# Performance work log

Measured on AMD Instinct MI355X. Metric: run time of the kernel, lower is better.

Reference implementation:

```python
import jax, jax.numpy as jnp
import numpy as np

B, S, D = 2, 2048, 512
P, T, MAP_H = 13, 5, 64


def setup_inputs() -> dict:
    key = jax.random.key(0)
    ks = jax.random.split(key, 8)
    s = 0.02
    return {
        "hidden_states": jax.random.normal(ks[0], (B, S, D), jnp.float32),
        "ln_gamma": jnp.ones((D,), jnp.float32),
        "ln_beta": jnp.zeros((D,), jnp.float32),
        "W_in": jax.random.normal(ks[1], (D, P * D), jnp.float32) * s,
        "b_in": jnp.zeros((P * D,), jnp.float32),
        "W_map1": jax.random.normal(ks[2], (D, MAP_H), jnp.float32) * s,
        "b_map1": jnp.zeros((MAP_H,), jnp.float32),
        "W_map2": jax.random.normal(ks[3], (MAP_H, T), jnp.float32) * s,
        "b_map2": jnp.zeros((T,), jnp.float32),
        "log_tau": jnp.linspace(0.0, 4.0, T).astype(jnp.float32),
        "mix": jax.random.normal(ks[4], (P, T), jnp.float32) / float(P * T),
        "W_out": jax.random.normal(ks[5], (D, D), jnp.float32) * s,
        "b_out": jnp.zeros((D,), jnp.float32),
        "scale": jnp.float32(1e-3),
        "h_prev": jnp.zeros((B, P, T, D), jnp.float32),
        "position_offset": 0,
    }


def _forward(hidden_states, ln_gamma, ln_beta, W_in, b_in, W_map1, b_map1,
             W_map2, b_map2, log_tau, mix, W_out, b_out, scale, h_prev):
    b, s_len, d = hidden_states.shape
    p, t = mix.shape
    # pre-norm (LayerNorm, eps=1e-5)
    mu = jnp.mean(hidden_states, -1, keepdims=True)
    var = jnp.var(hidden_states, -1, keepdims=True)
    xn = (hidden_states - mu) * jax.lax.rsqrt(var + 1e-5) * ln_gamma + ln_beta
    # per-protofilament input drive: [B,S,P,D]
    u = (xn @ W_in + b_in).reshape(b, s_len, p, d)
    # liquid (input-dependent) decay per time scale: [B,S,T]
    gate = jax.nn.sigmoid(jnp.tanh(xn @ W_map1 + b_map1) @ W_map2 + b_map2)
    alpha = jnp.exp(-gate / jnp.exp(log_tau))  # [B,S,T]

    def step(h, inp):
        u_t, a_t = inp                      # [B,P,D], [B,T]
        a = a_t[:, None, :, None]           # broadcast over P and D
        h = a * h + (1.0 - a) * u_t[:, :, None, :]   # [B,P,T,D]
        y = jnp.einsum('bptd,pt->bd', h, mix)        # mix protofilaments/time scales
        return h, y

    _, ys = jax.lax.scan(step, h_prev,
                         (jnp.moveaxis(u, 1, 0), jnp.moveaxis(alpha, 1, 0)))
    mt_out = jnp.moveaxis(ys, 0, 1) @ W_out + b_out  # [B,S,D]
    return hidden_states + scale * mt_out


def reference(hidden_states, ln_gamma, ln_beta, W_in, b_in, W_map1, b_map1,
              W_map2, b_map2, log_tau, mix, W_out, b_out, scale, h_prev,
              position_offset):
    return _forward(hidden_states, ln_gamma, ln_beta, W_in, b_in, W_map1,
                    b_map1, W_map2, b_map2, log_tau, mix, W_out, b_out,
                    scale, h_prev)
```

## Files before the change

### kernel.cpp

```cpp
#include <hip/hip_runtime.h>
#include <hip/hip_bf16.h>
#include <stdint.h>

#define BB 2
#define SS 2048
#define DD 512
#define PP 13
#define TT 5
#define MH 64
#define MM (BB*SS)
#define NV (TT*DD)
#define KK 512
#define CHUNK 16
#define NCH (SS/CHUNK)

typedef __attribute__((ext_vector_type(4))) float f32x4;
typedef __attribute__((ext_vector_type(8))) short s8v;
typedef unsigned int u32;
typedef __attribute__((address_space(3))) u32 lds_u32_t;
typedef __attribute__((address_space(1))) const u32 glb_u32_t;

__device__ __forceinline__ float bf2f(unsigned short u){
  union { unsigned int i; float f; } c; c.i = ((unsigned int)u) << 16; return c.f;
}
__device__ __forceinline__ unsigned short f2bf(float f){
  union { float f; unsigned int i; } c; c.f = f;
  unsigned int x = c.i;
  unsigned int r = (x + 0x7fffu + ((x >> 16) & 1u)) >> 16;
  return (unsigned short)r;
}
__device__ __forceinline__ void gld16(unsigned short* l, const unsigned short* g){
  __builtin_amdgcn_global_load_lds((glb_u32_t*)g, (lds_u32_t*)l, 16, 0, 0);
}

__global__ __launch_bounds__(256) void k_prep_ln(
    const float* __restrict__ hs,
    const float* __restrict__ gamma, const float* __restrict__ beta,
    const float* __restrict__ W_in, const float* __restrict__ b_in,
    const float* __restrict__ mix,  const float* __restrict__ W_out,
    const float* __restrict__ W1,
    unsigned short* __restrict__ xn_bf,
    unsigned short* __restrict__ W_vT, float* __restrict__ b_v,
    unsigned short* __restrict__ W_outT, unsigned short* __restrict__ W1T)
{
  int blk = blockIdx.x;
  if (blk < 1024){
    int tid = threadIdx.x;
    int lane = tid & 63;
    int row = blk*4 + (tid>>6);
    const float* x = hs + (size_t)row*DD + lane*8;
    float4 v0 = *(const float4*)x;
    float4 v1 = *(const float4*)(x+4);
    float s  = v0.x+v0.y+v0.z+v0.w + v1.x+v1.y+v1.z+v1.w;
    float sq = v0.x*v0.x+v0.y*v0.y+v0.z*v0.z+v0.w*v0.w
             + v1.x*v1.x+v1.y*v1.y+v1.z*v1.z+v1.w*v1.w;
    #pragma unroll
    for (int o=32;o>0;o>>=1){ s += __shfl_xor(s,o); sq += __shfl_xor(sq,o); }
    float mu   = s  * (1.f/DD);
    float var  = sq * (1.f/DD) - mu*mu;
    float rstd = rsqrtf(var + 1e-5f);
    float4 g0 = *(const float4*)(gamma + lane*8);
    float4 g1 = *(const float4*)(gamma + lane*8 + 4);
    float4 b0 = *(const float4*)(beta  + lane*8);
    float4 b1 = *(const float4*)(beta  + lane*8 + 4);
    union { unsigned short us[8]; uint4 u; } pk;
    pk.us[0] = f2bf((v0.x-mu)*rstd*g0.x + b0.x);
    pk.us[1] = f2bf((v0.y-mu)*rstd*g0.y + b0.y);
    pk.us[2] = f2bf((v0.z-mu)*rstd*g0.z + b0.z);
    pk.us[3] = f2bf((v0.w-mu)*rstd*g0.w + b0.w);
    pk.us[4] = f2bf((v1.x-mu)*rstd*g1.x + b1.x);
    pk.us[5] = f2bf((v1.y-mu)*rstd*g1.y + b1.y);
    pk.us[6] = f2bf((v1.z-mu)*rstd*g1.z + b1.z);
    pk.us[7] = f2bf((v1.w-mu)*rstd*g1.w + b1.w);
    *(uint4*)(xn_bf + (size_t)row*DD + lane*8) = pk.u;
  } else if (blk < 1152){
    int idx = (blk-1024) * 256 + threadIdx.x;
    int d  = idx & (DD-1);
    int k0 = idx >> 9;
    float mx[PP][TT];
    #pragma unroll
    for (int p=0;p<PP;++p)
      #pragma unroll
      for (int t=0;t<TT;++t) mx[p][t] = mix[p*TT+t];
    float acc[TT][8];
    #pragma unroll
    for (int t=0;t<TT;++t)
      #pragma unroll
      for (int j=0;j<8;++j) acc[t][j] = 0.f;
    #pragma unroll
    for (int j=0;j<8;++j){
      int k = k0*8 + j;
      const float* wrow = W_in + (size_t)k * (PP*DD) + d;
      #pragma unroll
      for (int p=0;p<PP;++p){
        float w = wrow[p*DD];
        #pragma unroll
        for (int t=0;t<TT;++t) acc[t][j] += mx[p][t]*w;
      }
    }
    #pragma unroll
    for (int t=0;t<TT;++t){
      union { unsigned short us[8]; uint4 u; } pk;
      #pragma unroll
      for (int j=0;j<8;++j) pk.us[j] = f2bf(acc[t][j]);
      *(uint4*)(W_vT + ((size_t)(t*DD+d))*KK + k0*8) = pk.u;
    }
    if (k0 == 0){
      #pragma unroll
      for (int t=0;t<TT;++t){
        float s = 0.f;
        #pragma unroll
        for (int p=0;p<PP;++p) s += mx[p][t]*b_in[p*DD+d];
        b_v[t*DD+d] = s;
      }
    }
  } else if (blk < 1280){
    int idx = (blk-1152)*256 + threadIdx.x;
    int n  = idx & (DD-1);
    int k0 = idx >> 9;
    union { unsigned short us[8]; uint4 u; } pk;
    #pragma unroll
    for (int j=0;j<8;++j) pk.us[j] = f2bf(W_out[(size_t)(k0*8+j)*DD + n]);
    *(uint4*)(W_outT + (size_t)n*KK + k0*8) = pk.u;
  } else {
    int idx = (blk-1280)*256 + threadIdx.x;
    int n  = idx >> 6;
    int k0 = idx & 63;
    union { unsigned short us[8]; uint4 u; } pk;
    #pragma unroll
    for (int j=0;j<8;++j) pk.us[j] = f2bf(W1[(size_t)(k0*8+j)*MH + n]);
    *(uint4*)(W1T + (size_t)n*KK + k0*8) = pk.u;
  }
}

__global__ __launch_bounds__(256) void k_gate(
    const unsigned short* __restrict__ xn,
    const unsigned short* __restrict__ W1T,
    const float* __restrict__ b1, const float* __restrict__ W2,
    const float* __restrict__ b2, const float* __restrict__ ltau,
    float* __restrict__ alpha)
{
  __shared__ unsigned short lA[2][64*32];
  __shared__ unsigned short lB[2][64*32];
  int bm = blockIdx.x;
  int tid = threadIdx.x, lane = tid & 63, w = tid >> 6;
  int lr = lane & 15, kq = lane >> 4;
  const uint8_t* gA = (const uint8_t*)(xn  + (size_t)(bm*64 + w*16 + (lane>>2))*KK) + (lane&3)*16;
  const uint8_t* gB = (const uint8_t*)(W1T + (size_t)(        w*16 + (lane>>2))*KK) + (lane&3)*16;
  f32x4 acc[4];
  #pragma unroll
  for (int ni=0;ni<4;++ni) acc[ni] = (f32x4){0.f,0.f,0.f,0.f};

  auto stage = [&](int buf, int kt){
    int off = kt*64;
    gld16(&lA[buf][(w*16)*32], (const unsigned short*)(gA + off));
    gld16(&lB[buf][(w*16)*32], (const unsigned short*)(gB + off));
  };
  auto compute = [&](int buf){
    union { uint4 u; s8v v; } af, bfr[4];
    af.u = *(const uint4*)&lA[buf][(w*16+lr)*32 + kq*8];
    #pragma unroll
    for (int ni=0;ni<4;++ni) bfr[ni].u = *(const uint4*)&lB[buf][(ni*16+lr)*32 + kq*8];
    #pragma unroll
    for (int ni=0;ni<4;++ni)
      acc[ni] = __builtin_amdgcn_mfma_f32_16x16x32_bf16(af.v, bfr[ni].v, acc[ni], 0,0,0);
  };

  stage(0, 0);
  __syncthreads();
  #pragma unroll
  for (int kt=1; kt<16; ++kt){
    stage(kt&1, kt);
    compute((kt&1)^1);
    __syncthreads();
  }
  compute(1);

  float z1[4][4];
  #pragma unroll
  for (int ni=0;ni<4;++ni){
    float bb = b1[ni*16+lr];
    #pragma unroll
    for (int r=0;r<4;++r) z1[r][ni] = tanhf(acc[ni][r] + bb);
  }
  float et[TT];
  #pragma unroll
  for (int t=0;t<TT;++t) et[t] = expf(-ltau[t]);
  float a[4][TT];
  #pragma unroll
  for (int t=0;t<TT;++t){
    float w2[4];
    #pragma unroll
    for (int ni=0;ni<4;++ni) w2[ni] = W2[(ni*16+lr)*TT + t];
    #pragma unroll
    for (int r=0;r<4;++r){
      float p = z1[r][0]*w2[0] + z1[r][1]*w2[1] + z1[r][2]*w2[2] + z1[r][3]*w2[3];
      #pragma unroll
      for (int o=8;o>0;o>>=1) p += __shfl_xor(p, o);
      float z2 = p + b2[t];
      float gate = 1.f/(1.f + expf(-z2));
      a[r][t] = expf(-gate * et[t]);
    }
  }
  if (lr < TT){
    int t = lr;
    #pragma unroll
    for (int r=0;r<4;++r){
      int row = bm*64 + w*16 + kq*4 + r;
      alpha[(size_t)row*TT + t] = a[r][t];
    }
  }
}

template<int BN, int NDIM, bool OUTEPI>
__global__ __launch_bounds__(256) void k_gemm(
    const unsigned short* __restrict__ A,
    const unsigned short* __restrict__ Bt,
    const float* __restrict__ bias,
    const float* __restrict__ hidden,
    const float* __restrict__ scale_p,
    float* __restrict__ outF,
    unsigned short* __restrict__ outBf)
{
  constexpr int NI  = (BN == 128) ? 4 : 2;
  constexpr int WNT = BN / 2;
  __shared__ unsigned short lA[2][128*32];
  __shared__ unsigned short lB[2][BN*32];
  int bn = blockIdx.x, bm = blockIdx.y;
  int tid  = threadIdx.x;
  int lane = tid & 63;
  int w    = tid >> 6;
  int wm = w >> 1, wn = w & 1;
  f32x4 acc[4][NI];
  #pragma unroll
  for (int i=0;i<4;++i)
    #pragma unroll
    for (int j=0;j<NI;++j) acc[i][j] = (f32x4){0.f,0.f,0.f,0.f};

  const uint8_t* gA = (const uint8_t*)(A + (size_t)(bm*128 + w*32 + (lane>>2))*KK) + (lane&3)*16;
  const uint8_t* gB;
  if constexpr (BN == 128) gB = (const uint8_t*)(Bt + (size_t)(bn*BN + w*32 + (lane>>2))*KK) + (lane&3)*16;
  else                     gB = (const uint8_t*)(Bt + (size_t)(bn*BN + w*16 + (lane>>2))*KK) + (lane&3)*16;
  int lr = lane & 15, kq = lane >> 4;

  auto stage = [&](int buf, int kt){
    int off = kt*64;
    gld16(&lA[buf][(w*32)*32],    (const unsigned short*)(gA + off));
    gld16(&lA[buf][(w*32+16)*32], (const unsigned short*)(gA + (size_t)16*KK*2 + off));
    if constexpr (BN == 128){
      gld16(&lB[buf][(w*32)*32],    (const unsigned short*)(gB + off));
      gld16(&lB[buf][(w*32+16)*32], (const unsigned short*)(gB + (size_t)16*KK*2 + off));
    } else {
      gld16(&lB[buf][(w*16)*32],    (const unsigned short*)(gB + off));
    }
  };
  auto compute = [&](int buf){
    union { uint4 u; s8v v; } af[4], bfr[NI];
    #pragma unroll
    for (int mi=0;mi<4;++mi) af[mi].u  = *(const uint4*)&lA[buf][(wm*64+mi*16+lr)*32 + kq*8];
    #pragma unroll
    for (int ni=0;ni<NI;++ni) bfr[ni].u = *(const uint4*)&lB[buf][(wn*WNT+ni*16+lr)*32 + kq*8];
    #pragma unroll
    for (int mi=0;mi<4;++mi)
      #pragma unroll
      for (int ni=0;ni<NI;++ni)
        acc[mi][ni] = __builtin_amdgcn_mfma_f32_16x16x32_bf16(af[mi].v, bfr[ni].v, acc[mi][ni], 0,0,0);
  };

  stage(0, 0);
  __syncthreads();
  #pragma unroll
  for (int kt=1; kt<16; ++kt){
    stage(kt&1, kt);
    compute((kt&1)^1);
    __syncthreads();
  }
  compute(1);

  float sc = 0.f;
  if constexpr (OUTEPI) sc = *scale_p;
  #pragma unroll
  for (int mi=0;mi<4;++mi){
    #pragma unroll
    for (int ni=0;ni<NI;++ni){
      int row = bm*128 + wm*64 + mi*16 + kq*4;
      int col = bn*BN  + wn*WNT + ni*16 + lr;
      float bs = bias[col];
      f32x4 c = acc[mi][ni];
      #pragma unroll
      for (int r=0;r<4;++r){
        float val = c[r] + bs;
        size_t off = (size_t)(row+r)*NDIM + col;
        if constexpr (OUTEPI) outF[off] = hidden[off] + sc*val;
        else                  outBf[off] = f2bf(val);
      }
    }
  }
}

__global__ __launch_bounds__(320) void k_scan_a(
    const float* __restrict__ alpha,
    unsigned short* __restrict__ vg,
    float* __restrict__ L, float* __restrict__ PA)
{
  int blk = blockIdx.x;
  int c = blk & (NCH-1), b = blk >> 7;
  int tid = threadIdx.x;
  int t  = tid >> 6;
  int d8 = tid & 63;
  __shared__ float sAl[CHUNK*TT];
  if (tid < CHUNK*TT) sAl[tid] = alpha[(size_t)(b*SS + c*CHUNK)*TT + tid];
  __syncthreads();
  unsigned short* vp = vg + (size_t)(b*SS + c*CHUNK)*NV + t*DD + d8*8;
  uint4 vv[CHUNK];
  #pragma unroll
  for (int s2=0;s2<CHUNK;++s2) vv[s2] = *(const uint4*)(vp + (size_t)s2*NV);
  float g[8];
  #pragma unroll
  for (int j=0;j<8;++j) g[j] = 0.f;
  float pa = 1.f;
  #pragma unroll
  for (int s2=0;s2<CHUNK;++s2){
    float a = sAl[s2*TT+t], om = 1.f - a;
    const unsigned short* pv = (const unsigned short*)&vv[s2];
    union { unsigned short us[8]; uint4 u; } o;
    #pragma unroll
    for (int j=0;j<8;++j){ g[j] = a*g[j] + om*bf2f(pv[j]); o.us[j] = f2bf(g[j]); }
    *(uint4*)(vp + (size_t)s2*NV) = o.u;
    pa *= a;
  }
  float* Lp = L + ((size_t)(b*TT+t)*NCH + c)*DD + d8*8;
  *(float4*)Lp     = (float4){g[0],g[1],g[2],g[3]};
  *(float4*)(Lp+4) = (float4){g[4],g[5],g[6],g[7]};
  if (d8 == 0) PA[(size_t)(b*TT+t)*NCH + c] = pa;
}

__global__ __launch_bounds__(512) void k_scan_b(
    const float* __restrict__ mix,
    const float* __restrict__ h_prev,
    const float* __restrict__ PA,
    const float* __restrict__ L,
    float* __restrict__ Gc)
{
  int blk = blockIdx.x;
  int t = blk % TT, b = blk / TT;
  int d = threadIdx.x;
  __shared__ float sP[NCH];
  if (d < NCH) sP[d] = PA[(size_t)(b*TT+t)*NCH + d];
  __syncthreads();
  float carry = 0.f;
  #pragma unroll
  for (int p=0;p<PP;++p)
    carry += mix[p*TT+t] * h_prev[((size_t)(b*PP+p)*TT + t)*DD + d];
  const float* Lp = L  + (size_t)(b*TT+t)*NCH*DD + d;
  float*       gc = Gc + (size_t)(b*TT+t)*NCH*DD + d;
  float buf[8], nbuf[8];
  #pragma unroll
  for (int j=0;j<8;++j) buf[j] = Lp[(size_t)j*DD];
  for (int c0=0;c0<NCH;c0+=8){
    if (c0+8 < NCH){
      #pragma unroll
      for (int j=0;j<8;++j) nbuf[j] = Lp[(size_t)(c0+8+j)*DD];
    }
    #pragma unroll
    for (int j=0;j<8;++j){
      gc[(size_t)(c0+j)*DD] = carry;
      carry = sP[c0+j]*carry + buf[j];
    }
    #pragma unroll
    for (int j=0;j<8;++j) buf[j] = nbuf[j];
  }
}

__global__ __launch_bounds__(256) void k_scan_c(
    const float* __restrict__ alpha,
    const unsigned short* __restrict__ g_loc,
    const float* __restrict__ Gc,
    unsigned short* __restrict__ ybf)
{
  int blk = blockIdx.x;
  int c = blk & (NCH-1), b = blk >> 7;
  int tid = threadIdx.x;
  int s4 = tid >> 6;
  int d8 = tid & 63;
  __shared__ float sAl[CHUNK*TT];
  if (tid < CHUNK*TT) sAl[tid] = alpha[(size_t)(b*SS + c*CHUNK)*TT + tid];
  __syncthreads();
  float ca[TT][8];
  #pragma unroll
  for (int t=0;t<TT;++t){
    const float* gp = Gc + ((size_t)(b*TT+t)*NCH + c)*DD + d8*8;
    float4 c0 = *(const float4*)gp;
    float4 c1 = *(const float4*)(gp+4);
    ca[t][0]=c0.x; ca[t][1]=c0.y; ca[t][2]=c0.z; ca[t][3]=c0.w;
    ca[t][4]=c1.x; ca[t][5]=c1.y; ca[t][6]=c1.z; ca[t][7]=c1.w;
  }
  float pr[TT];
  #pragma unroll
  for (int t=0;t<TT;++t){
    float p = 1.f;
    for (int j=0;j<s4*4;++j) p *= sAl[j*TT+t];
    pr[t] = p;
  }
  const unsigned short* gl = g_loc + (size_t)(b*SS + c*CHUNK)*NV + d8*8;
  unsigned short* yp = ybf + (size_t)(b*SS + c*CHUNK)*DD + d8*8;
  #pragma unroll
  for (int i=0;i<4;++i){
    int s2 = s4*4 + i;
    float y[8];
    #pragma unroll
    for (int j=0;j<8;++j) y[j] = 0.f;
    #pragma unroll
    for (int t=0;t<TT;++t){
      pr[t] *= sAl[s2*TT+t];
      uint4 gv = *(const uint4*)(gl + (size_t)s2*NV + t*DD);
      const unsigned short* gp = (const unsigned short*)&gv;
      #pragma unroll
      for (int j=0;j<8;++j) y[j] += bf2f(gp[j]) + pr[t]*ca[t][j];
    }
    union { unsigned short us[8]; uint4 u; } o;
    #pragma unroll
    for (int j=0;j<8;++j) o.us[j] = f2bf(y[j]);
    *(uint4*)(yp + (size_t)s2*DD) = o.u;
  }
}

extern "C" void kernel_launch(void* const* d_in, const int* in_sizes, int n_in,
                              void* d_out, int out_size, void* d_ws, size_t ws_size,
                              hipStream_t stream)
{
  (void)in_sizes; (void)n_in; (void)out_size; (void)ws_size;
  const float* hs     = (const float*)d_in[0];
  const float* gamma  = (const float*)d_in[1];
  const float* beta   = (const float*)d_in[2];
  const float* W_in   = (const float*)d_in[3];
  const float* b_in   = (const float*)d_in[4];
  const float* W1     = (const float*)d_in[5];
  const float* b1     = (const float*)d_in[6];
  const float* W2     = (const float*)d_in[7];
  const float* b2     = (const float*)d_in[8];
  const float* ltau   = (const float*)d_in[9];
  const float* mix    = (const float*)d_in[10];
  const float* W_out  = (const float*)d_in[11];
  const float* b_out  = (const float*)d_in[12];
  const float* scale  = (const float*)d_in[13];
  const float* h_prev = (const float*)d_in[14];
  float* out = (float*)d_out;

  uint8_t* w = (uint8_t*)d_ws;
  unsigned short* xn   = (unsigned short*)(w);
  unsigned short* WvT  = (unsigned short*)(w + 4194304);
  unsigned short* WoT  = (unsigned short*)(w + 6815744);
  float* alphaB        = (float*)(w + 7340032);
  float* b_v           = (float*)(w + 7421952);
  float* PA            = (float*)(w + 7432192);
  float* L             = (float*)(w + 7437312);
  float* Gc            = (float*)(w + 10058752);
  unsigned short* vg   = (unsigned short*)(w + 12680192);
  unsigned short* ybf  = (unsigned short*)(w + 33651712);
  unsigned short* W1T  = ybf;

  hipLaunchKernelGGL(k_prep_ln, dim3(1296), dim3(256), 0, stream,
                     hs, gamma, beta, W_in, b_in, mix, W_out, W1,
                     xn, WvT, b_v, WoT, W1T);
  hipLaunchKernelGGL(k_gate, dim3(MM/64), dim3(256), 0, stream, xn, W1T, b1, W2, b2, ltau, alphaB);
  hipLaunchKernelGGL((k_gemm<128,NV,false>), dim3(NV/128, MM/128), dim3(256), 0, stream,
                     xn, WvT, b_v, nullptr, nullptr, nullptr, vg);
  hipLaunchKernelGGL(k_scan_a, dim3(BB*NCH), dim3(320), 0, stream, alphaB, vg, L, PA);
  hipLaunchKernelGGL(k_scan_b, dim3(BB*TT), dim3(512), 0, stream, mix, h_prev, PA, L, Gc);
  hipLaunchKernelGGL(k_scan_c, dim3(BB*NCH), dim3(256), 0, stream, alphaB, vg, Gc, ybf);
  hipLaunchKernelGGL((k_gemm<64,DD,true>), dim3(DD/64, MM/128), dim3(256), 0, stream,
                     ybf, WoT, b_out, hs, scale, out, nullptr);
}
```

Before: 82.95 us.

## Fuse gate MLP into input GEMM and pre-reduce scan outputs over time scales

The separate gate kernel is removed. Its first layer (W1) is appended as extra columns of the input-drive weight matrix, zero-padded to a multiple of 128. The last column-block of the big GEMM then computes tanh, the second layer, sigmoid and alpha in its epilogue. Separately, scan_a now sums the five time-scale local states in LDS and writes a single bf16 row per position, so scan_c reads one row instead of five, cutting global traffic. This saves one launch and a pass over xn, at the cost of extra zero-padded GEMM work, an LDS buffer in scan_a, and extra syncs.

```diff
diff --git a/kernel.cpp b/kernel.cpp
--- a/kernel.cpp
+++ b/kernel.cpp
@@ -10,6 +10,7 @@
 #define MH 64
 #define MM (BB*SS)
 #define NV (TT*DD)
+#define NX 2688
 #define KK 512
 #define CHUNK 16
 #define NCH (SS/CHUNK)
@@ -38,10 +39,10 @@
     const float* __restrict__ gamma, const float* __restrict__ beta,
     const float* __restrict__ W_in, const float* __restrict__ b_in,
     const float* __restrict__ mix,  const float* __restrict__ W_out,
-    const float* __restrict__ W1,
+    const float* __restrict__ W1,   const float* __restrict__ b1,
     unsigned short* __restrict__ xn_bf,
     unsigned short* __restrict__ W_vT, float* __restrict__ b_v,
-    unsigned short* __restrict__ W_outT, unsigned short* __restrict__ W1T)
+    unsigned short* __restrict__ W_outT)
 {
   int blk = blockIdx.x;
   if (blk < 1024){
@@ -62,16 +63,16 @@
     float4 g0 = *(const float4*)(gamma + lane*8);
     float4 g1 = *(const float4*)(gamma + lane*8 + 4);
     float4 b0 = *(const float4*)(beta  + lane*8);
-    float4 b1 = *(const float4*)(beta  + lane*8 + 4);
+    float4 b1v = *(const float4*)(beta + lane*8 + 4);
     union { unsigned short us[8]; uint4 u; } pk;
     pk.us[0] = f2bf((v0.x-mu)*rstd*g0.x + b0.x);
     pk.us[1] = f2bf((v0.y-mu)*rstd*g0.y + b0.y);
     pk.us[2] = f2bf((v0.z-mu)*rstd*g0.z + b0.z);
     pk.us[3] = f2bf((v0.w-mu)*rstd*g0.w + b0.w);
-    pk.us[4] = f2bf((v1.x-mu)*rstd*g1.x + b1.x);
-    pk.us[5] = f2bf((v1.y-mu)*rstd*g1.y + b1.y);
-    pk.us[6] = f2bf((v1.z-mu)*rstd*g1.z + b1.z);
-    pk.us[7] = f2bf((v1.w-mu)*rstd*g1.w + b1.w);
+    pk.us[4] = f2bf((v1.x-mu)*rstd*g1.x + b1v.x);
+    pk.us[5] = f2bf((v1.y-mu)*rstd*g1.y + b1v.y);
+    pk.us[6] = f2bf((v1.z-mu)*rstd*g1.z + b1v.z);
+    pk.us[7] = f2bf((v1.w-mu)*rstd*g1.w + b1v.w);
     *(uint4*)(xn_bf + (size_t)row*DD + lane*8) = pk.u;
   } else if (blk < 1152){
     int idx = (blk-1024) * 256 + threadIdx.x;
@@ -122,97 +123,26 @@
     #pragma unroll
     for (int j=0;j<8;++j) pk.us[j] = f2bf(W_out[(size_t)(k0*8+j)*DD + n]);
     *(uint4*)(W_outT + (size_t)n*KK + k0*8) = pk.u;
-  } else {
+  } else if (blk < 1296){
     int idx = (blk-1280)*256 + threadIdx.x;
     int n  = idx >> 6;
     int k0 = idx & 63;
     union { unsigned short us[8]; uint4 u; } pk;
     #pragma unroll
     for (int j=0;j<8;++j) pk.us[j] = f2bf(W1[(size_t)(k0*8+j)*MH + n]);
-    *(uint4*)(W1T + (size_t)n*KK + k0*8) = pk.u;
-  }
-}
-
-__global__ __launch_bounds__(256) void k_gate(
-    const unsigned short* __restrict__ xn,
-    const unsigned short* __restrict__ W1T,
-    const float* __restrict__ b1, const float* __restrict__ W2,
-    const float* __restrict__ b2, const float* __restrict__ ltau,
-    float* __restrict__ alpha)
-{
-  __shared__ unsigned short lA[2][64*32];
-  __shared__ unsigned short lB[2][64*32];
-  int bm = blockIdx.x;
-  int tid = threadIdx.x, lane = tid & 63, w = tid >> 6;
-  int lr = lane & 15, kq = lane >> 4;
-  const uint8_t* gA = (const uint8_t*)(xn  + (size_t)(bm*64 + w*16 + (lane>>2))*KK) + (lane&3)*16;
-  const uint8_t* gB = (const uint8_t*)(W1T + (size_t)(        w*16 + (lane>>2))*KK) + (lane&3)*16;
-  f32x4 acc[4];
-  #pragma unroll
-  for (int ni=0;ni<4;++ni) acc[ni] = (f32x4){0.f,0.f,0.f,0.f};
-
-  auto stage = [&](int buf, int kt){
-    int off = kt*64;
-    gld16(&lA[buf][(w*16)*32], (const unsigned short*)(gA + off));
-    gld16(&lB[buf][(w*16)*32], (const unsigned short*)(gB + off));
-  };
-  auto compute = [&](int buf){
-    union { uint4 u; s8v v; } af, bfr[4];
-    af.u = *(const uint4*)&lA[buf][(w*16+lr)*32 + kq*8];
-    #pragma unroll
-    for (int ni=0;ni<4;++ni) bfr[ni].u = *(const uint4*)&lB[buf][(ni*16+lr)*32 + kq*8];
-    #pragma unroll
-    for (int ni=0;ni<4;++ni)
-      acc[ni] = __builtin_amdgcn_mfma_f32_16x16x32_bf16(af.v, bfr[ni].v, acc[ni], 0,0,0);
-  };
-
-  stage(0, 0);
-  __syncthreads();
-  #pragma unroll
-  for (int kt=1; kt<16; ++kt){
-    stage(kt&1, kt);
-    compute((kt&1)^1);
-    __syncthreads();
-  }
-  compute(1);
-
-  float z1[4][4];
-  #pragma unroll
-  for (int ni=0;ni<4;++ni){
-    float bb = b1[ni*16+lr];
-    #pragma unroll
-    for (int r=0;r<4;++r) z1[r][ni] = tanhf(acc[ni][r] + bb);
-  }
-  float et[TT];
-  #pragma unroll
-  for (int t=0;t<TT;++t) et[t] = expf(-ltau[t]);
-  float a[4][TT];
-  #pragma unroll
-  for (int t=0;t<TT;++t){
-    float w2[4];
-    #pragma unroll
-    for (int ni=0;ni<4;++ni) w2[ni] = W2[(ni*16+lr)*TT + t];
-    #pragma unroll
-    for (int r=0;r<4;++r){
-      float p = z1[r][0]*w2[0] + z1[r][1]*w2[1] + z1[r][2]*w2[2] + z1[r][3]*w2[3];
-      #pragma unroll
-      for (int o=8;o>0;o>>=1) p += __shfl_xor(p, o);
-      float z2 = p + b2[t];
-      float gate = 1.f/(1.f + expf(-z2));
-      a[r][t] = expf(-gate * et[t]);
-    }
-  }
-  if (lr < TT){
-    int t = lr;
-    #pragma unroll
-    for (int r=0;r<4;++r){
-      int row = bm*64 + w*16 + kq*4 + r;
-      alpha[(size_t)row*TT + t] = a[r][t];
-    }
-  }
-}
-
-template<int BN, int NDIM, bool OUTEPI>
+    *(uint4*)(W_vT + (size_t)(NV+n)*KK + k0*8) = pk.u;
+    if (k0 == 0) b_v[NV+n] = b1[n];
+  } else {
+    int idx = (blk-1296)*256 + threadIdx.x;
+    int n  = idx >> 6;
+    int k0 = idx & 63;
+    uint4 z; z.x=z.y=z.z=z.w=0u;
+    *(uint4*)(W_vT + (size_t)(NV+MH+n)*KK + k0*8) = z;
+    if (blk == 1296 && threadIdx.x < MH) b_v[NV+MH+threadIdx.x] = 0.f;
+  }
+}
+
+template<int BN, int NDIM, bool OUTEPI, bool GATE>
 __global__ __launch_bounds__(256) void k_gemm(
     const unsigned short* __restrict__ A,
     const unsigned short* __restrict__ Bt,
@@ -220,7 +150,11 @@
     const float* __restrict__ hidden,
     const float* __restrict__ scale_p,
     float* __restrict__ outF,
-    unsigned short* __restrict__ outBf)
+    unsigned short* __restrict__ outBf,
+    const float* __restrict__ W2,
+    const float* __restrict__ b2,
+    const float* __restrict__ ltau,
+    float* __restrict__ alphaOut)
 {
   constexpr int NI  = (BN == 128) ? 4 : 2;
   constexpr int WNT = BN / 2;
@@ -277,6 +211,46 @@
   }
   compute(1);
 
+  if constexpr (GATE){
+    if (bn == (int)gridDim.x - 1){
+      if (wn != 0) return;
+      float et[TT];
+      #pragma unroll
+      for (int t=0;t<TT;++t) et[t] = expf(-ltau[t]);
+      #pragma unroll
+      for (int mi=0;mi<4;++mi){
+        float z1v[4][4];
+        #pragma unroll
+        for (int ni=0;ni<4;++ni){
+          float bb = bias[bn*BN + ni*16 + lr];
+          #pragma unroll
+          for (int r=0;r<4;++r) z1v[ni][r] = tanhf(acc[mi][ni][r] + bb);
+        }
+        #pragma unroll
+        for (int t=0;t<TT;++t){
+          float w2v[4];
+          #pragma unroll
+          for (int ni=0;ni<4;++ni) w2v[ni] = W2[(ni*16+lr)*TT + t];
+          #pragma unroll
+          for (int r=0;r<4;++r){
+            float p = z1v[0][r]*w2v[0] + z1v[1][r]*w2v[1]
+                    + z1v[2][r]*w2v[2] + z1v[3][r]*w2v[3];
+            p += __shfl_xor(p, 1);
+            p += __shfl_xor(p, 2);
+            p += __shfl_xor(p, 4);
+            p += __shfl_xor(p, 8);
+            if (lr == t){
+              float gate = 1.f/(1.f + expf(-(p + b2[t])));
+              int row = bm*128 + wm*64 + mi*16 + kq*4 + r;
+              alphaOut[(size_t)row*TT + t] = expf(-gate * et[t]);
+            }
+          }
+        }
+      }
+      return;
+    }
+  }
+
   float sc = 0.f;
   if constexpr (OUTEPI) sc = *scale_p;
   #pragma unroll
@@ -300,8 +274,9 @@
 
 __global__ __launch_bounds__(320) void k_scan_a(
     const float* __restrict__ alpha,
-    unsigned short* __restrict__ vg,
-    float* __restrict__ L, float* __restrict__ PA)
+    const unsigned short* __restrict__ v,
+    float* __restrict__ L, float* __restrict__ PA,
+    unsigned short* __restrict__ yloc)
 {
   int blk = blockIdx.x;
   int c = blk & (NCH-1), b = blk >> 7;
@@ -309,25 +284,51 @@
   int t  = tid >> 6;
   int d8 = tid & 63;
   __shared__ float sAl[CHUNK*TT];
+  __shared__ unsigned short yl[TT][8][DD];
   if (tid < CHUNK*TT) sAl[tid] = alpha[(size_t)(b*SS + c*CHUNK)*TT + tid];
   __syncthreads();
-  unsigned short* vp = vg + (size_t)(b*SS + c*CHUNK)*NV + t*DD + d8*8;
-  uint4 vv[CHUNK];
-  #pragma unroll
-  for (int s2=0;s2<CHUNK;++s2) vv[s2] = *(const uint4*)(vp + (size_t)s2*NV);
+  const unsigned short* vp = v + (size_t)(b*SS + c*CHUNK)*NV + t*DD + d8*8;
   float g[8];
   #pragma unroll
   for (int j=0;j<8;++j) g[j] = 0.f;
   float pa = 1.f;
   #pragma unroll
-  for (int s2=0;s2<CHUNK;++s2){
-    float a = sAl[s2*TT+t], om = 1.f - a;
-    const unsigned short* pv = (const unsigned short*)&vv[s2];
-    union { unsigned short us[8]; uint4 u; } o;
-    #pragma unroll
-    for (int j=0;j<8;++j){ g[j] = a*g[j] + om*bf2f(pv[j]); o.us[j] = f2bf(g[j]); }
-    *(uint4*)(vp + (size_t)s2*NV) = o.u;
-    pa *= a;
+  for (int half=0; half<2; ++half){
+    uint4 vv[8];
+    #pragma unroll
+    for (int s=0;s<8;++s) vv[s] = *(const uint4*)(vp + (size_t)(half*8+s)*NV);
+    #pragma unroll
+    for (int s=0;s<8;++s){
+      float a = sAl[(half*8+s)*TT+t], om = 1.f - a;
+      const unsigned short* pv = (const unsigned short*)&vv[s];
+      union { unsigned short us[8]; uint4 u; } o;
+      #pragma unroll
+      for (int j=0;j<8;++j){ g[j] = a*g[j] + om*bf2f(pv[j]); o.us[j] = f2bf(g[j]); }
+      *(uint4*)&yl[t][s][d8*8] = o.u;
+      pa *= a;
+    }
+    __syncthreads();
+    if (t < 4){
+      #pragma unroll
+      for (int ii=0; ii<2; ++ii){
+        int s = t*2 + ii;
+        float y[8];
+        #pragma unroll
+        for (int j=0;j<8;++j) y[j] = 0.f;
+        #pragma unroll
+        for (int tt=0;tt<TT;++tt){
+          uint4 gv = *(const uint4*)&yl[tt][s][d8*8];
+          const unsigned short* gp = (const unsigned short*)&gv;
+          #pragma unroll
+          for (int j=0;j<8;++j) y[j] += bf2f(gp[j]);
+        }
+        union { unsigned short us[8]; uint4 u; } o;
+        #pragma unroll
+        for (int j=0;j<8;++j) o.us[j] = f2bf(y[j]);
+        *(uint4*)(yloc + (size_t)(b*SS + c*CHUNK + half*8 + s)*DD + d8*8) = o.u;
+      }
+    }
+    __syncthreads();
   }
   float* Lp = L + ((size_t)(b*TT+t)*NCH + c)*DD + d8*8;
   *(float4*)Lp     = (float4){g[0],g[1],g[2],g[3]};
@@ -374,7 +375,7 @@
 
 __global__ __launch_bounds__(256) void k_scan_c(
     const float* __restrict__ alpha,
-    const unsigned short* __restrict__ g_loc,
+    const unsigned short* __restrict__ yloc,
     const float* __restrict__ Gc,
     unsigned short* __restrict__ ybf)
 {
@@ -402,26 +403,26 @@
     for (int j=0;j<s4*4;++j) p *= sAl[j*TT+t];
     pr[t] = p;
   }
-  const unsigned short* gl = g_loc + (size_t)(b*SS + c*CHUNK)*NV + d8*8;
-  unsigned short* yp = ybf + (size_t)(b*SS + c*CHUNK)*DD + d8*8;
+  const unsigned short* yp = yloc + (size_t)(b*SS + c*CHUNK)*DD + d8*8;
+  unsigned short* op = ybf + (size_t)(b*SS + c*CHUNK)*DD + d8*8;
   #pragma unroll
   for (int i=0;i<4;++i){
     int s2 = s4*4 + i;
+    uint4 yv = *(const uint4*)(yp + (size_t)s2*DD);
+    const unsigned short* yq = (const unsigned short*)&yv;
     float y[8];
     #pragma unroll
-    for (int j=0;j<8;++j) y[j] = 0.f;
+    for (int j=0;j<8;++j) y[j] = bf2f(yq[j]);
     #pragma unroll
     for (int t=0;t<TT;++t){
       pr[t] *= sAl[s2*TT+t];
-      uint4 gv = *(const uint4*)(gl + (size_t)s2*NV + t*DD);
-      const unsigned short* gp = (const unsigned short*)&gv;
-      #pragma unroll
-      for (int j=0;j<8;++j) y[j] += bf2f(gp[j]) + pr[t]*ca[t][j];
+      #pragma unroll
+      for (int j=0;j<8;++j) y[j] += pr[t]*ca[t][j];
     }
     union { unsigned short us[8]; uint4 u; } o;
     #pragma unroll
     for (int j=0;j<8;++j) o.us[j] = f2bf(y[j]);
-    *(uint4*)(yp + (size_t)s2*DD) = o.u;
+    *(uint4*)(op + (size_t)s2*DD) = o.u;
   }
 }
 
@@ -449,26 +450,27 @@
 
   uint8_t* w = (uint8_t*)d_ws;
   unsigned short* xn   = (unsigned short*)(w);
-  unsigned short* WvT  = (unsigned short*)(w + 4194304);
-  unsigned short* WoT  = (unsigned short*)(w + 6815744);
-  float* alphaB        = (float*)(w + 7340032);
-  float* b_v           = (float*)(w + 7421952);
-  float* PA            = (float*)(w + 7432192);
-  float* L             = (float*)(w + 7437312);
-  float* Gc            = (float*)(w + 10058752);
-  unsigned short* vg   = (unsigned short*)(w + 12680192);
-  unsigned short* ybf  = (unsigned short*)(w + 33651712);
-  unsigned short* W1T  = ybf;
-
-  hipLaunchKernelGGL(k_prep_ln, dim3(1296), dim3(256), 0, stream,
-                     hs, gamma, beta, W_in, b_in, mix, W_out, W1,
-                     xn, WvT, b_v, WoT, W1T);
-  hipLaunchKernelGGL(k_gate, dim3(MM/64), dim3(256), 0, stream, xn, W1T, b1, W2, b2, ltau, alphaB);
-  hipLaunchKernelGGL((k_gemm<128,NV,false>), dim3(NV/128, MM/128), dim3(256), 0, stream,
-                     xn, WvT, b_v, nullptr, nullptr, nullptr, vg);
-  hipLaunchKernelGGL(k_scan_a, dim3(BB*NCH), dim3(320), 0, stream, alphaB, vg, L, PA);
+  unsigned short* WvTX = (unsigned short*)(w + 4194304);
+  unsigned short* WoT  = (unsigned short*)(w + 6946816);
+  float* alphaB        = (float*)(w + 7471104);
+  float* b_vX          = (float*)(w + 7553024);
+  float* PA            = (float*)(w + 7563776);
+  float* L             = (float*)(w + 7568896);
+  float* Gc            = (float*)(w + 10190336);
+  unsigned short* vg   = (unsigned short*)(w + 12811776);
+  unsigned short* ybf  = (unsigned short*)(w + 33783296);
+  unsigned short* yloc = xn;
+
+  hipLaunchKernelGGL(k_prep_ln, dim3(1312), dim3(256), 0, stream,
+                     hs, gamma, beta, W_in, b_in, mix, W_out, W1, b1,
+                     xn, WvTX, b_vX, WoT);
+  hipLaunchKernelGGL((k_gemm<128,NV,false,true>), dim3(NX/128, MM/128), dim3(256), 0, stream,
+                     xn, WvTX, b_vX, nullptr, nullptr, nullptr, vg,
+                     W2, b2, ltau, alphaB);
+  hipLaunchKernelGGL(k_scan_a, dim3(BB*NCH), dim3(320), 0, stream, alphaB, vg, L, PA, yloc);
   hipLaunchKernelGGL(k_scan_b, dim3(BB*TT), dim3(512), 0, stream, mix, h_prev, PA, L, Gc);
-  hipLaunchKernelGGL(k_scan_c, dim3(BB*NCH), dim3(256), 0, stream, alphaB, vg, Gc, ybf);
-  hipLaunchKernelGGL((k_gemm<64,DD,true>), dim3(DD/64, MM/128), dim3(256), 0, stream,
-                     ybf, WoT, b_out, hs, scale, out, nullptr);
-}
+  hipLaunchKernelGGL(k_scan_c, dim3(BB*NCH), dim3(256), 0, stream, alphaB, yloc, Gc, ybf);
+  hipLaunchKernelGGL((k_gemm<64,DD,true,false>), dim3(DD/64, MM/128), dim3(256), 0, stream,
+                     ybf, WoT, b_out, hs, scale, out, nullptr,
+                     nullptr, nullptr, nullptr, nullptr);
+}
```

Measured after the change: 110.8 us. 33.6% more time.
